# Kernel tuning notes

Hardware: AMD Instinct MI355X
Metric: run time of the kernel (lower is better)

Reference implementation:

```python
import jax, jax.numpy as jnp
import numpy as np

B, C, H, W, D = 4, 64, 64, 192, 24


def setup_inputs() -> dict:
    key = jax.random.key(0)
    ks = jax.random.split(key, 8)
    x = jax.random.normal(ks[0], (B, C, H, W), dtype=jnp.float32)
    y = jax.random.normal(ks[1], (B, C, H, W), dtype=jnp.float32)
    # disparity coordinate samples: pixel x-coordinates in [0, W-1]
    d1 = jax.random.uniform(ks[2], (B, D, H, W), dtype=jnp.float32) * (W - 1.0)
    d2 = jax.random.uniform(ks[3], (B, D, H, W), dtype=jnp.float32) * (W - 1.0)
    s = 1.0 / np.sqrt(C)
    qw = jax.random.normal(ks[4], (C, C), dtype=jnp.float32) * s
    qb = jax.random.normal(ks[5], (C,), dtype=jnp.float32) * 0.01
    kw = jax.random.normal(ks[6], (C, C), dtype=jnp.float32) * s
    kb = jax.random.normal(ks[7], (C,), dtype=jnp.float32) * 0.01
    return {"x": x, "y": y, "disp_range_samples1": d1, "disp_range_samples2": d2,
            "ndisp": D, "qw": qw, "qb": qb, "kw": kw, "kb": kb}


def _conv1x1(x, w, b):
    return jnp.einsum('oi,bihw->bohw', w, x) + b[None, :, None, None]


def _cost_volume(Q, K, disp_x):
    """mean_c( Q * grid_sample(K, bilinear, zeros, align_corners=False) ).
    Q,K: [B,C,H,W]; disp_x: [B,D,H,W] pixel x-coords. Returns [B,D,H,W]."""
    b, c, h, w = K.shape
    # torch grid_sample(align_corners=False) unnormalization of
    # coords = pix/((dim-1)/2)-1  ->  pix*dim/(dim-1) - 0.5
    xs = disp_x * (w / (w - 1.0)) - 0.5                      # [B,D,H,W]
    ys_row = jnp.arange(h, dtype=xs.dtype) * (h / (h - 1.0)) - 0.5
    ys = jnp.broadcast_to(ys_row[None, None, :, None], xs.shape)
    x0 = jnp.floor(xs)
    y0 = jnp.floor(ys)
    tx = xs - x0
    ty = ys - y0
    x0i = x0.astype(jnp.int32)
    y0i = y0.astype(jnp.int32)

    def corner(dy, dx, wgt):
        yi = y0i + dy
        xi = x0i + dx
        valid = ((yi >= 0) & (yi < h) & (xi >= 0) & (xi < w)).astype(Q.dtype)
        yc = jnp.clip(yi, 0, h - 1)
        xc = jnp.clip(xi, 0, w - 1)
        # per-batch gather: [C,H,W] indexed by [D,H,W] -> [C,D,H,W]
        g = jax.vmap(lambda im, yy, xx: im[:, yy, xx])(K, yc, xc)  # [B,C,D,H,W]
        return jnp.einsum('bchw,bcdhw->bdhw', Q, g * (wgt * valid)[:, None])

    cost = (corner(0, 0, (1.0 - ty) * (1.0 - tx)) +
            corner(0, 1, (1.0 - ty) * tx) +
            corner(1, 0, ty * (1.0 - tx)) +
            corner(1, 1, ty * tx))
    return cost / c


def reference(x, y, disp_range_samples1, disp_range_samples2, ndisp, qw, qb, kw, kb):
    assert ndisp == disp_range_samples1.shape[1]
    Q1 = _conv1x1(x, qw, qb)
    K1 = _conv1x1(y, kw, kb)
    cost1 = _cost_volume(Q1, K1, disp_range_samples1)
    Q2 = _conv1x1(y, qw, qb)
    K2 = _conv1x1(x, kw, kb)
    cost2 = _cost_volume(Q2, K2, disp_range_samples2)
    return (cost1, cost2)
```

## Files before the change

kernel.cpp:

```cpp
#include <hip/hip_runtime.h>
#include <stdint.h>

#define BB 4
#define CC 64
#define HH 64
#define WW 192
#define DD 24
#define HWQ (HH * WW)
#define PIX (BB * HWQ)

typedef __attribute__((ext_vector_type(8))) short short8;
typedef __attribute__((ext_vector_type(4))) float floatx4;

__device__ __forceinline__ float bf1(uint16_t u) {
    union { uint32_t i; float f; } c; c.i = ((uint32_t)u) << 16; return c.f;
}
__device__ __forceinline__ uint16_t f2bf(float f) {
    union { float f; uint32_t i; } c; c.f = f;
    uint32_t u = c.i;
    return (uint16_t)((u + 0x7fffu + ((u >> 16) & 1u)) >> 16);
}

#define A_SHORTS ((size_t)2 * PIX * CC)
#define S_F32OFF 4240

__global__ __launch_bounds__(64) void prep_kernel(
    const float* __restrict__ qw, const float* __restrict__ qb,
    const float* __restrict__ kw, const float* __restrict__ kb,
    float* __restrict__ fws) {
    const int bid = blockIdx.x;
    const int j   = threadIdx.x;
    if (bid < 64) {
        float acc = 0.f;
        for (int c = 0; c < CC; c++)
            acc = fmaf(qw[c * CC + bid], kw[c * CC + j], acc);
        fws[bid * 64 + j] = acc;
    } else if (bid == 64) {
        float bt = 0.f;
        for (int c = 0; c < CC; c++) bt = fmaf(qb[c], kw[c * CC + j], bt);
        fws[4096 + j] = bt;
        if (j == 0) {
            float g = 0.f;
            for (int c = 0; c < CC; c++) g = fmaf(qb[c], kb[c], g);
            fws[4224] = g;
        }
    } else {
        float al = 0.f;
        for (int c = 0; c < CC; c++) al = fmaf(qw[c * CC + j], kb[c], al);
        fws[4160 + j] = al;
    }
}

__global__ __launch_bounds__(256) void convA_kernel(
    const float* __restrict__ x, const float* __restrict__ y,
    const float* __restrict__ fws, uint16_t* __restrict__ A) {
    const int v = blockIdx.y;
    const float* src = v ? y : x;
    const float* G     = fws;
    const float* beta  = fws + 4096;
    const float* alpha = fws + 4160;
    const float* gamma = fws + 4224;
    float* s = const_cast<float*>(fws) + S_F32OFF;

    __shared__ float wt[64][64];
    __shared__ float bs[64], al[64];
    __shared__ float gm;
    const int tid = threadIdx.y * 64 + threadIdx.x;
    for (int idx = tid; idx < 4096; idx += 256) wt[idx >> 6][idx & 63] = G[idx];
    if (tid < 64) { bs[tid] = beta[tid]; al[tid] = alpha[tid]; }
    if (tid == 64) gm = *gamma;
    __syncthreads();

    const int pix0 = blockIdx.x * 256 + threadIdx.x * 4;
    const int b    = pix0 / HWQ;
    const int hw0  = pix0 - b * HWQ;
    const int j0   = threadIdx.y * 16;

    float acc[4][16];
#pragma unroll
    for (int p = 0; p < 4; p++)
#pragma unroll
        for (int k = 0; k < 16; k++) acc[p][k] = bs[j0 + k];
    float sac[4] = {gm, gm, gm, gm};

    const float* sp = src + (size_t)b * CC * HWQ + hw0;
#pragma unroll 4
    for (int i = 0; i < 64; i++) {
        float4 raw = *reinterpret_cast<const float4*>(sp + (size_t)i * HWQ);
        const float* wr = &wt[i][j0];
        const float av = al[i];
        sac[0] = fmaf(raw.x, av, sac[0]);
        sac[1] = fmaf(raw.y, av, sac[1]);
        sac[2] = fmaf(raw.z, av, sac[2]);
        sac[3] = fmaf(raw.w, av, sac[3]);
#pragma unroll
        for (int k = 0; k < 16; k++) {
            float wv = wr[k];
            acc[0][k] = fmaf(raw.x, wv, acc[0][k]);
            acc[1][k] = fmaf(raw.y, wv, acc[1][k]);
            acc[2][k] = fmaf(raw.z, wv, acc[2][k]);
            acc[3][k] = fmaf(raw.w, wv, acc[3][k]);
        }
    }

    uint16_t* dstv = A + (size_t)v * PIX * CC;
#pragma unroll
    for (int p = 0; p < 4; p++) {
        uint32_t pk[8];
#pragma unroll
        for (int k = 0; k < 8; k++)
            pk[k] = (uint32_t)f2bf(acc[p][2 * k]) | ((uint32_t)f2bf(acc[p][2 * k + 1]) << 16);
        uint16_t* dp = dstv + (size_t)(pix0 + p) * CC + j0;
        uint4 lo; lo.x = pk[0]; lo.y = pk[1]; lo.z = pk[2]; lo.w = pk[3];
        uint4 hi; hi.x = pk[4]; hi.y = pk[5]; hi.z = pk[6]; hi.w = pk[7];
        *reinterpret_cast<uint4*>(dp)     = lo;
        *reinterpret_cast<uint4*>(dp + 8) = hi;
    }
    if (threadIdx.y == 0) {
        float4 sv; sv.x = sac[0]; sv.y = sac[1]; sv.z = sac[2]; sv.w = sac[3];
        *reinterpret_cast<float4*>(s + (size_t)v * PIX + pix0) = sv;
    }
}

__global__ __launch_bounds__(1024) void cost_kernel(
    const float* __restrict__ x, const float* __restrict__ y,
    const float* __restrict__ disp1, const float* __restrict__ disp2,
    const uint16_t* __restrict__ A, const float* __restrict__ fws,
    float* __restrict__ out) {
    const int h = blockIdx.x;
    const int b = blockIdx.y;
    const int v = blockIdx.z;

    const float*    Yv   = v ? x : y;
    const float*    disp = v ? disp2 : disp1;
    const uint16_t* Ab   = A + ((size_t)v * PIX + (size_t)b * HWQ + h * WW) * CC;
    const float*    sb   = fws + S_F32OFF + (size_t)v * PIX + (size_t)b * HWQ + h * WW;

    const float ys  = (float)h * (float)(64.0 / 63.0) - 0.5f;
    const float y0f = floorf(ys);
    const float ty  = ys - y0f;
    const int   y0  = (int)y0f;
    const int   y1  = y0 + 1;
    const float vy0 = (y0 >= 0 && y0 < HH) ? 1.f : 0.f;
    const float vy1 = (y1 >= 0 && y1 < HH) ? 1.f : 0.f;
    const int   y0c = min(max(y0, 0), HH - 1);
    const int   y1c = min(max(y1, 0), HH - 1);
    const float ey0 = (1.f - ty) * vy0;
    const float ey1 = ty * vy1;
    const float eysum = ey0 + ey1;

    __shared__ uint16_t Yc[192 * 68];
    __shared__ uint16_t Pt[96 * 196];

    const int tid  = threadIdx.x;
    const int wave = tid >> 6;
    const int lane = tid & 63;
    const int lq   = lane >> 4;
    const int ln   = lane & 15;

    const float* Yb0 = Yv + ((size_t)b * CC * HH + y0c) * WW;
    const float* Yb1 = Yv + ((size_t)b * CC * HH + y1c) * WW;
#pragma unroll
    for (int k = 0; k < 3; k++) {
        const int cg = wave;
        const int xx = k * 64 + lane;
        uint32_t pk[2];
#pragma unroll
        for (int half = 0; half < 2; half++) {
            uint32_t pv = 0;
#pragma unroll
            for (int j = 0; j < 2; j++) {
                const int c = cg * 4 + half * 2 + j;
                const float v0 = Yb0[(size_t)c * HH * WW + xx];
                const float v1 = Yb1[(size_t)c * HH * WW + xx];
                const float cb = fmaf(ey1, v1, ey0 * v0);
                pv |= ((uint32_t)f2bf(cb)) << (16 * j);
            }
            pk[half] = pv;
        }
        *reinterpret_cast<uint2*>(&Yc[xx * 68 + cg * 4]) = *reinterpret_cast<uint2*>(pk);
    }
    __syncthreads();

    const float cx = (float)(192.0 / 191.0);
    const float inv_c = 1.f / 64.f;

    for (int half = 0; half < 2; half++) {
        if (wave < 12) {
            const int mcl = wave >> 1;
            const uint16_t* ar = Ab + (size_t)(half * 96 + mcl * 16 + ln) * CC + lq * 8;
            short8 a0 = *reinterpret_cast<const short8*>(ar);
            short8 a1 = *reinterpret_cast<const short8*>(ar + 32);
#pragma unroll
            for (int i = 0; i < 6; i++) {
                const int nt = (wave & 1) * 6 + i;
                const int Rb = nt * 16;
                const uint16_t* yrow = &Yc[(Rb + ln) * 68 + lq * 8];
                short8 b0, b1;
                *reinterpret_cast<uint2*>(&b0)       = *reinterpret_cast<const uint2*>(yrow);
                *(reinterpret_cast<uint2*>(&b0) + 1) = *reinterpret_cast<const uint2*>(yrow + 4);
                *reinterpret_cast<uint2*>(&b1)       = *reinterpret_cast<const uint2*>(yrow + 32);
                *(reinterpret_cast<uint2*>(&b1) + 1) = *reinterpret_cast<const uint2*>(yrow + 36);
                floatx4 acc = {0.f, 0.f, 0.f, 0.f};
                acc = __builtin_amdgcn_mfma_f32_16x16x32_bf16(a0, b0, acc, 0, 0, 0);
                acc = __builtin_amdgcn_mfma_f32_16x16x32_bf16(a1, b1, acc, 0, 0, 0);
                const int pcol = Rb + ln;
                const int wl   = mcl * 16 + lq * 4;
                Pt[(wl + 0) * 196 + pcol] = f2bf(acc[0]);
                Pt[(wl + 1) * 196 + pcol] = f2bf(acc[1]);
                Pt[(wl + 2) * 196 + pcol] = f2bf(acc[2]);
                Pt[(wl + 3) * 196 + pcol] = f2bf(acc[3]);
            }
        }
        __syncthreads();

        for (int o = tid; o < 96 * DD; o += 1024) {
            const int wl = o % 96;
            const int d  = o / 96;
            const int w  = half * 96 + wl;
            const float dsv = disp[((size_t)(b * DD + d) * HH + h) * WW + w];
            const float xs  = dsv * cx - 0.5f;
            const float x0f = floorf(xs);
            const float tx  = xs - x0f;
            const int   x0  = (int)x0f;
            const int   x1  = x0 + 1;
            const float vx0 = (x0 >= 0 && x0 < WW) ? 1.f : 0.f;
            const float vx1 = (x1 >= 0 && x1 < WW) ? 1.f : 0.f;
            const int   x0c = min(max(x0, 0), WW - 1);
            const int   x1c = min(max(x1, 0), WW - 1);
            const float wx0 = (1.f - tx) * vx0;
            const float wx1 = tx * vx1;
            const float pc0 = bf1(Pt[wl * 196 + x0c]);
            const float pc1 = bf1(Pt[wl * 196 + x1c]);
            const float res = wx0 * pc0 + wx1 * pc1 + sb[w] * (eysum * (wx0 + wx1));
            out[(((size_t)(v * BB + b) * DD + d) * HH + h) * WW + w] = res * inv_c;
        }
        __syncthreads();
    }
}

extern "C" void kernel_launch(void* const* d_in, const int* in_sizes, int n_in,
                              void* d_out, int out_size, void* d_ws, size_t ws_size,
                              hipStream_t stream) {
    const float* x  = (const float*)d_in[0];
    const float* y  = (const float*)d_in[1];
    const float* d1 = (const float*)d_in[2];
    const float* d2 = (const float*)d_in[3];
    const float* qw = (const float*)d_in[5];
    const float* qb = (const float*)d_in[6];
    const float* kw = (const float*)d_in[7];
    const float* kb = (const float*)d_in[8];

    uint16_t* A   = (uint16_t*)d_ws;
    float*    fws = (float*)((uint16_t*)d_ws + A_SHORTS);
    float*    out = (float*)d_out;

    prep_kernel<<<dim3(66), dim3(64), 0, stream>>>(qw, qb, kw, kb, fws);
    convA_kernel<<<dim3(PIX / 256, 2), dim3(64, 4), 0, stream>>>(x, y, fws, A);
    cost_kernel<<<dim3(HH, BB, 2), dim3(1024), 0, stream>>>(x, y, d1, d2, A, fws, out);
}
```

Measured before the change: 133.5 us.

## Move 1x1 conv projection onto bf16 MFMA and spread cost-volume MFMA tiles across waves

The convA kernel now stages the input pixels and the fused weight matrix as bf16 in shared memory and computes the projection with 16x16x32 bf16 MFMA instructions instead of scalar fp32 FMAs. The per-pixel alpha dot product is taken from the staged bf16 tile. In the cost kernel, all 16 waves now share the 72 MFMA tiles instead of only 12 waves doing them, shared-memory row pitches are padded to reduce bank conflicts, and the trailing barrier is skipped on the last half. The cost is extra bf16 rounding of the input and weights, which adds numerical error, plus scattered 2-byte global stores of the conv output.

New measurement: 159.9 us. +19.7%, slower.

```diff
diff --git a/kernel.cpp b/kernel.cpp
--- a/kernel.cpp
+++ b/kernel.cpp
@@ -51,74 +51,79 @@
     }
 }
 
-__global__ __launch_bounds__(256) void convA_kernel(
+__global__ __launch_bounds__(128) void convA_kernel(
     const float* __restrict__ x, const float* __restrict__ y,
     const float* __restrict__ fws, uint16_t* __restrict__ A) {
     const int v = blockIdx.y;
     const float* src = v ? y : x;
-    const float* G     = fws;
-    const float* beta  = fws + 4096;
-    const float* alpha = fws + 4160;
-    const float* gamma = fws + 4224;
     float* s = const_cast<float*>(fws) + S_F32OFF;
 
-    __shared__ float wt[64][64];
-    __shared__ float bs[64], al[64];
-    __shared__ float gm;
-    const int tid = threadIdx.y * 64 + threadIdx.x;
-    for (int idx = tid; idx < 4096; idx += 256) wt[idx >> 6][idx & 63] = G[idx];
-    if (tid < 64) { bs[tid] = beta[tid]; al[tid] = alpha[tid]; }
-    if (tid == 64) gm = *gamma;
-    __syncthreads();
-
-    const int pix0 = blockIdx.x * 256 + threadIdx.x * 4;
+    __shared__ uint16_t Xt[128 * 70];
+    __shared__ uint16_t Gt[64 * 70];
+    __shared__ float    bsS[64], alS[64];
+    __shared__ float    gmS;
+
+    const int tid  = threadIdx.x;
+    const int pix0 = blockIdx.x * 128;
     const int b    = pix0 / HWQ;
     const int hw0  = pix0 - b * HWQ;
-    const int j0   = threadIdx.y * 16;
-
-    float acc[4][16];
-#pragma unroll
-    for (int p = 0; p < 4; p++)
-#pragma unroll
-        for (int k = 0; k < 16; k++) acc[p][k] = bs[j0 + k];
-    float sac[4] = {gm, gm, gm, gm};
+
+    for (int idx = tid; idx < 4096; idx += 128) {
+        const int c = idx >> 6, j = idx & 63;
+        Gt[j * 70 + c] = f2bf(fws[idx]);
+    }
+    if (tid < 64) { bsS[tid] = fws[4096 + tid]; alS[tid] = fws[4160 + tid]; }
+    if (tid == 64) gmS = fws[4224];
 
     const float* sp = src + (size_t)b * CC * HWQ + hw0;
-#pragma unroll 4
-    for (int i = 0; i < 64; i++) {
-        float4 raw = *reinterpret_cast<const float4*>(sp + (size_t)i * HWQ);
-        const float* wr = &wt[i][j0];
-        const float av = al[i];
-        sac[0] = fmaf(raw.x, av, sac[0]);
-        sac[1] = fmaf(raw.y, av, sac[1]);
-        sac[2] = fmaf(raw.z, av, sac[2]);
-        sac[3] = fmaf(raw.w, av, sac[3]);
-#pragma unroll
-        for (int k = 0; k < 16; k++) {
-            float wv = wr[k];
-            acc[0][k] = fmaf(raw.x, wv, acc[0][k]);
-            acc[1][k] = fmaf(raw.y, wv, acc[1][k]);
-            acc[2][k] = fmaf(raw.z, wv, acc[2][k]);
-            acc[3][k] = fmaf(raw.w, wv, acc[3][k]);
-        }
-    }
-
-    uint16_t* dstv = A + (size_t)v * PIX * CC;
-#pragma unroll
-    for (int p = 0; p < 4; p++) {
-        uint32_t pk[8];
-#pragma unroll
-        for (int k = 0; k < 8; k++)
-            pk[k] = (uint32_t)f2bf(acc[p][2 * k]) | ((uint32_t)f2bf(acc[p][2 * k + 1]) << 16);
-        uint16_t* dp = dstv + (size_t)(pix0 + p) * CC + j0;
-        uint4 lo; lo.x = pk[0]; lo.y = pk[1]; lo.z = pk[2]; lo.w = pk[3];
-        uint4 hi; hi.x = pk[4]; hi.y = pk[5]; hi.z = pk[6]; hi.w = pk[7];
-        *reinterpret_cast<uint4*>(dp)     = lo;
-        *reinterpret_cast<uint4*>(dp + 8) = hi;
-    }
-    if (threadIdx.y == 0) {
-        float4 sv; sv.x = sac[0]; sv.y = sac[1]; sv.z = sac[2]; sv.w = sac[3];
-        *reinterpret_cast<float4*>(s + (size_t)v * PIX + pix0) = sv;
+    for (int it = tid; it < 1024; it += 128) {
+        const int pg = it & 31;
+        const int cp = it >> 5;
+        float4 r0 = *reinterpret_cast<const float4*>(sp + (size_t)(2 * cp)     * HWQ + pg * 4);
+        float4 r1 = *reinterpret_cast<const float4*>(sp + (size_t)(2 * cp + 1) * HWQ + pg * 4);
+        const int base = (pg * 4) * 70 + 2 * cp;
+        *reinterpret_cast<uint32_t*>(&Xt[base])           = (uint32_t)f2bf(r0.x) | ((uint32_t)f2bf(r1.x) << 16);
+        *reinterpret_cast<uint32_t*>(&Xt[base + 70])      = (uint32_t)f2bf(r0.y) | ((uint32_t)f2bf(r1.y) << 16);
+        *reinterpret_cast<uint32_t*>(&Xt[base + 140])     = (uint32_t)f2bf(r0.z) | ((uint32_t)f2bf(r1.z) << 16);
+        *reinterpret_cast<uint32_t*>(&Xt[base + 210])     = (uint32_t)f2bf(r0.w) | ((uint32_t)f2bf(r1.w) << 16);
+    }
+    __syncthreads();
+
+    const int wave = tid >> 6;
+    const int lane = tid & 63;
+    const int lq   = lane >> 4;
+    const int ln   = lane & 15;
+
+    uint16_t* Abase = A + (size_t)v * PIX * CC;
+    for (int t = wave * 16; t < wave * 16 + 16; t++) {
+        const int mt = t >> 2, nt = t & 3;
+        const uint16_t* xr = &Xt[(mt * 16 + ln) * 70 + lq * 8];
+        const uint16_t* gr = &Gt[(nt * 16 + ln) * 70 + lq * 8];
+        short8 a0, a1, b0, b1;
+        *reinterpret_cast<uint2*>(&a0)       = *reinterpret_cast<const uint2*>(xr);
+        *(reinterpret_cast<uint2*>(&a0) + 1) = *reinterpret_cast<const uint2*>(xr + 4);
+        *reinterpret_cast<uint2*>(&a1)       = *reinterpret_cast<const uint2*>(xr + 32);
+        *(reinterpret_cast<uint2*>(&a1) + 1) = *reinterpret_cast<const uint2*>(xr + 36);
+        *reinterpret_cast<uint2*>(&b0)       = *reinterpret_cast<const uint2*>(gr);
+        *(reinterpret_cast<uint2*>(&b0) + 1) = *reinterpret_cast<const uint2*>(gr + 4);
+        *reinterpret_cast<uint2*>(&b1)       = *reinterpret_cast<const uint2*>(gr + 32);
+        *(reinterpret_cast<uint2*>(&b1) + 1) = *reinterpret_cast<const uint2*>(gr + 36);
+        const float bias = bsS[nt * 16 + ln];
+        floatx4 acc = {bias, bias, bias, bias};
+        acc = __builtin_amdgcn_mfma_f32_16x16x32_bf16(a0, b0, acc, 0, 0, 0);
+        acc = __builtin_amdgcn_mfma_f32_16x16x32_bf16(a1, b1, acc, 0, 0, 0);
+        uint16_t* dp = Abase + (size_t)(pix0 + mt * 16 + lq * 4) * CC + nt * 16 + ln;
+        dp[0 * CC] = f2bf(acc[0]);
+        dp[1 * CC] = f2bf(acc[1]);
+        dp[2 * CC] = f2bf(acc[2]);
+        dp[3 * CC] = f2bf(acc[3]);
+    }
+
+    {
+        float sacc = gmS;
+        const uint16_t* xp = &Xt[tid * 70];
+        for (int c = 0; c < CC; c++) sacc = fmaf(alS[c], bf1(xp[c]), sacc);
+        s[(size_t)v * PIX + pix0 + tid] = sacc;
     }
 }
 
@@ -149,8 +154,8 @@
     const float ey1 = ty * vy1;
     const float eysum = ey0 + ey1;
 
-    __shared__ uint16_t Yc[192 * 68];
-    __shared__ uint16_t Pt[96 * 196];
+    __shared__ uint16_t Yc[192 * 70];
+    __shared__ uint16_t Pt[96 * 198];
 
     const int tid  = threadIdx.x;
     const int wave = tid >> 6;
@@ -178,7 +183,7 @@
             }
             pk[half] = pv;
         }
-        *reinterpret_cast<uint2*>(&Yc[xx * 68 + cg * 4]) = *reinterpret_cast<uint2*>(pk);
+        *reinterpret_cast<uint2*>(&Yc[xx * 70 + cg * 4]) = *reinterpret_cast<uint2*>(pk);
     }
     __syncthreads();
 
@@ -186,31 +191,28 @@
     const float inv_c = 1.f / 64.f;
 
     for (int half = 0; half < 2; half++) {
-        if (wave < 12) {
-            const int mcl = wave >> 1;
+        for (int t = wave; t < 72; t += 16) {
+            const int mcl = t / 12;
+            const int nt  = t - mcl * 12;
             const uint16_t* ar = Ab + (size_t)(half * 96 + mcl * 16 + ln) * CC + lq * 8;
             short8 a0 = *reinterpret_cast<const short8*>(ar);
             short8 a1 = *reinterpret_cast<const short8*>(ar + 32);
-#pragma unroll
-            for (int i = 0; i < 6; i++) {
-                const int nt = (wave & 1) * 6 + i;
-                const int Rb = nt * 16;
-                const uint16_t* yrow = &Yc[(Rb + ln) * 68 + lq * 8];
-                short8 b0, b1;
-                *reinterpret_cast<uint2*>(&b0)       = *reinterpret_cast<const uint2*>(yrow);
-                *(reinterpret_cast<uint2*>(&b0) + 1) = *reinterpret_cast<const uint2*>(yrow + 4);
-                *reinterpret_cast<uint2*>(&b1)       = *reinterpret_cast<const uint2*>(yrow + 32);
-                *(reinterpret_cast<uint2*>(&b1) + 1) = *reinterpret_cast<const uint2*>(yrow + 36);
-                floatx4 acc = {0.f, 0.f, 0.f, 0.f};
-                acc = __builtin_amdgcn_mfma_f32_16x16x32_bf16(a0, b0, acc, 0, 0, 0);
-                acc = __builtin_amdgcn_mfma_f32_16x16x32_bf16(a1, b1, acc, 0, 0, 0);
-                const int pcol = Rb + ln;
-                const int wl   = mcl * 16 + lq * 4;
-                Pt[(wl + 0) * 196 + pcol] = f2bf(acc[0]);
-                Pt[(wl + 1) * 196 + pcol] = f2bf(acc[1]);
-                Pt[(wl + 2) * 196 + pcol] = f2bf(acc[2]);
-                Pt[(wl + 3) * 196 + pcol] = f2bf(acc[3]);
-            }
+            const int Rb = nt * 16;
+            const uint16_t* yrow = &Yc[(Rb + ln) * 70 + lq * 8];
+            short8 b0, b1;
+            *reinterpret_cast<uint2*>(&b0)       = *reinterpret_cast<const uint2*>(yrow);
+            *(reinterpret_cast<uint2*>(&b0) + 1) = *reinterpret_cast<const uint2*>(yrow + 4);
+            *reinterpret_cast<uint2*>(&b1)       = *reinterpret_cast<const uint2*>(yrow + 32);
+            *(reinterpret_cast<uint2*>(&b1) + 1) = *reinterpret_cast<const uint2*>(yrow + 36);
+            floatx4 acc = {0.f, 0.f, 0.f, 0.f};
+            acc = __builtin_amdgcn_mfma_f32_16x16x32_bf16(a0, b0, acc, 0, 0, 0);
+            acc = __builtin_amdgcn_mfma_f32_16x16x32_bf16(a1, b1, acc, 0, 0, 0);
+            const int pcol = Rb + ln;
+            const int wl   = mcl * 16 + lq * 4;
+            Pt[(wl + 0) * 198 + pcol] = f2bf(acc[0]);
+            Pt[(wl + 1) * 198 + pcol] = f2bf(acc[1]);
+            Pt[(wl + 2) * 198 + pcol] = f2bf(acc[2]);
+            Pt[(wl + 3) * 198 + pcol] = f2bf(acc[3]);
         }
         __syncthreads();
 
@@ -230,12 +232,12 @@
             const int   x1c = min(max(x1, 0), WW - 1);
             const float wx0 = (1.f - tx) * vx0;
             const float wx1 = tx * vx1;
-            const float pc0 = bf1(Pt[wl * 196 + x0c]);
-            const float pc1 = bf1(Pt[wl * 196 + x1c]);
+            const float pc0 = bf1(Pt[wl * 198 + x0c]);
+            const float pc1 = bf1(Pt[wl * 198 + x1c]);
             const float res = wx0 * pc0 + wx1 * pc1 + sb[w] * (eysum * (wx0 + wx1));
             out[(((size_t)(v * BB + b) * DD + d) * HH + h) * WW + w] = res * inv_c;
         }
-        __syncthreads();
+        if (half == 0) __syncthreads();
     }
 }
 
@@ -256,6 +258,6 @@
     float*    out = (float*)d_out;
 
     prep_kernel<<<dim3(66), dim3(64), 0, stream>>>(qw, qb, kw, kb, fws);
-    convA_kernel<<<dim3(PIX / 256, 2), dim3(64, 4), 0, stream>>>(x, y, fws, A);
+    convA_kernel<<<dim3(PIX / 128, 2), dim3(128), 0, stream>>>(x, y, fws, A);
     cost_kernel<<<dim3(HH, BB, 2), dim3(1024), 0, stream>>>(x, y, d1, d2, A, fws, out);
 }
```
